# Optimization experiments

Hardware: AMD Instinct MI355X
Metric: run time of the kernel (lower is better)

Reference implementation:

```python
import jax, jax.numpy as jnp
import numpy as np

B, S, D, H = 2, 2048, 1024, 16
HD = D // H  # head_dim = 64


def setup_inputs() -> dict:
    key = jax.random.key(0)
    ks = jax.random.split(key, 11)
    s = 0.02  # keep projections well-scaled
    return {
        "Q": jax.random.normal(ks[0], (B, S, D), jnp.float32),
        "K": jax.random.normal(ks[1], (B, S, D), jnp.float32),
        "V": jax.random.normal(ks[2], (B, S, D), jnp.float32),
        "Wq": jax.random.normal(ks[3], (D, D), jnp.float32) * s,
        "bq": jax.random.normal(ks[4], (D,), jnp.float32) * s,
        "Wk": jax.random.normal(ks[5], (D, D), jnp.float32) * s,
        "bk": jax.random.normal(ks[6], (D,), jnp.float32) * s,
        "Wv": jax.random.normal(ks[7], (D, D), jnp.float32) * s,
        "bv": jax.random.normal(ks[8], (D,), jnp.float32) * s,
        "Wo": jax.random.normal(ks[9], (D, D), jnp.float32) * s,
        "bo": jax.random.normal(ks[10], (D,), jnp.float32) * s,
    }


def reference(Q, K, V, Wq, bq, Wk, bk, Wv, bv, Wo, bo):
    b, s, d = Q.shape
    # projections (torch Linear: x @ W.T + b)
    q = (Q @ Wq.T + bq).reshape(b, s, H, HD).transpose(0, 2, 1, 3)  # [B,H,S,HD]
    k = (K @ Wk.T + bk).reshape(b, s, H, HD).transpose(0, 2, 1, 3)
    v = (V @ Wv.T + bv).reshape(b, s, H, HD).transpose(0, 2, 1, 3)
    # scaled dot-product scores: [B,H,S,S]
    scale = 1.0 / jnp.sqrt(jnp.asarray(HD, q.dtype))
    scores = jnp.einsum("bhqd,bhkd->bhqk", q, k) * scale
    # module's explicit max-subtract before softmax
    scores = scores - jnp.max(scores, axis=-1, keepdims=True)
    attn = jax.nn.softmax(scores, axis=-1)
    # dropout p=0.0 (eval) -> identity; renormalize-after-dropout kept verbatim
    attn = attn / jnp.sum(attn, axis=-1, keepdims=True)
    ctx = jnp.einsum("bhqk,bhkd->bhqd", attn, v)  # [B,H,S,HD]
    ctx = ctx.transpose(0, 2, 1, 3).reshape(b, s, d)
    out = ctx @ Wo.T + bo
    return out
```

## Files before the change

kernel.cpp:

```cpp
#include <hip/hip_runtime.h>

#define SS 2048
#define SD 1024
#define SH 16
#define SHD 64
#define MROWS 4096
#define LOG2E 1.44269504088896340736f

typedef __attribute__((ext_vector_type(8))) short short8;
typedef __attribute__((ext_vector_type(4))) float floatx4;
typedef __attribute__((ext_vector_type(4))) unsigned short ushort4v;
typedef unsigned short u16;
typedef unsigned int u32;

#define AS1 __attribute__((address_space(1)))
#define AS3 __attribute__((address_space(3)))

__device__ inline u16 f2bf(float v) {
  u32 x = __builtin_bit_cast(u32, v);
  x = x + 0x7fffu + ((x >> 16) & 1u);
  return (u16)(x >> 16);
}

__global__ __launch_bounds__(256) void cast_all(
    const float* __restrict__ q, const float* __restrict__ k,
    const float* __restrict__ v, const float* __restrict__ wq,
    const float* __restrict__ wk, const float* __restrict__ wv,
    const float* __restrict__ wo, u16* __restrict__ out) {
  int i = blockIdx.x * 256 + threadIdx.x;
  const float* src;
  int idx;
  if (i < 3145728) {
    int a = i >> 20;
    src = (a == 0) ? q : ((a == 1) ? k : v);
    idx = i & 1048575;
  } else {
    int j = i - 3145728;
    int a = j >> 18;
    src = (a == 0) ? wq : ((a == 1) ? wk : ((a == 2) ? wv : wo));
    idx = j & 262143;
  }
  float4 f = ((const float4*)src)[idx];
  ushort4v o;
  o[0] = f2bf(f.x); o[1] = f2bf(f.y); o[2] = f2bf(f.z); o[3] = f2bf(f.w);
  ((ushort4v*)out)[i] = o;
}

__global__ __launch_bounds__(256, 3) void gemm_bt(
    const u16* __restrict__ Aall, const u16* __restrict__ Wall,
    const float* __restrict__ b0, const float* __restrict__ b1,
    const float* __restrict__ b2, u16* __restrict__ outb,
    float* __restrict__ outf, int mode, float qscale) {
  __shared__ u16 smem[16384];
  u16* lds_a = smem;
  u16* lds_w = smem + 8192;
  int z = blockIdx.z;
  const u16* A = Aall + (size_t)z * (MROWS * (size_t)SD);
  const u16* W = Wall + (size_t)z * (SD * (size_t)SD);
  const float* bias = (z == 0) ? b0 : ((z == 1) ? b1 : b2);
  float scale = (mode == 0 && z == 0) ? qscale : 1.0f;

  int tid = threadIdx.x;
  int lane = tid & 63, wave = tid >> 6;
  int l16 = lane & 15, quad = lane >> 4;
  int wm = (wave >> 1) * 64, wn = (wave & 1) * 64;
  int tm = blockIdx.y * 128, tn = blockIdx.x * 128;

  floatx4 acc[4][4];
  floatx4 zf = {0.f, 0.f, 0.f, 0.f};
#pragma unroll
  for (int r = 0; r < 4; r++)
#pragma unroll
    for (int c = 0; c < 4; c++) acc[r][c] = zf;

  const u16* pa[4];
  const u16* pw[4];
#pragma unroll
  for (int q = 0; q < 4; q++) {
    int srow = q * 32 + wave * 8 + (lane >> 3);
    int scol = (((lane & 7) ^ ((lane >> 3) & 7)) << 3);
    pa[q] = A + (size_t)(tm + srow) * SD + scol;
    pw[q] = W + (size_t)(tn + srow) * SD + scol;
  }

  for (int k0 = 0; k0 < SD; k0 += 64) {
#pragma unroll
    for (int q = 0; q < 4; q++) {
      __builtin_amdgcn_global_load_lds((const AS1 void*)pa[q],
          (AS3 void*)(AS3 u16*)&lds_a[(q * 32 + wave * 8) * 64], 16, 0, 0);
      __builtin_amdgcn_global_load_lds((const AS1 void*)pw[q],
          (AS3 void*)(AS3 u16*)&lds_w[(q * 32 + wave * 8) * 64], 16, 0, 0);
      pa[q] += 64; pw[q] += 64;
    }
    __syncthreads();
    short8 af[4][2], wf[4][2];
#pragma unroll
    for (int r = 0; r < 4; r++)
#pragma unroll
      for (int kk = 0; kk < 2; kk++)
        af[r][kk] = *(short8*)&lds_a[(wm + r * 16 + l16) * 64 +
                                     (((kk * 4 + quad) ^ (l16 & 7)) << 3)];
#pragma unroll
    for (int c = 0; c < 4; c++)
#pragma unroll
      for (int kk = 0; kk < 2; kk++)
        wf[c][kk] = *(short8*)&lds_w[(wn + c * 16 + l16) * 64 +
                                     (((kk * 4 + quad) ^ (l16 & 7)) << 3)];
#pragma unroll
    for (int r = 0; r < 4; r++)
#pragma unroll
      for (int c = 0; c < 4; c++) {
        acc[r][c] = __builtin_amdgcn_mfma_f32_16x16x32_bf16(af[r][0], wf[c][0], acc[r][c], 0, 0, 0);
        acc[r][c] = __builtin_amdgcn_mfma_f32_16x16x32_bf16(af[r][1], wf[c][1], acc[r][c], 0, 0, 0);
      }
    __syncthreads();
  }

  if (mode == 0) {
    u16* ob = outb + (size_t)z * (MROWS * (size_t)SD);
    if (z < 2) {
      u16* LT = smem;
#pragma unroll
      for (int r = 0; r < 4; r++) {
#pragma unroll
        for (int c = 0; c < 4; c++) {
          int feat = wn + c * 16 + l16;
          float bv = bias[tn + feat];
#pragma unroll
          for (int g = 0; g < 4; g++) {
            int key = wm + r * 16 + quad * 4 + g;
            float val = (acc[r][c][g] + bv) * scale;
            LT[key * 128 + ((((feat >> 3) ^ (key & 7)) << 3) | (feat & 7))] = f2bf(val);
          }
        }
      }
      __syncthreads();
      int bb = tm >> 11;
      int kt0 = (tm & 2047) >> 6;
#pragma unroll
      for (int i = 0; i < 8; i++) {
        int id = wave * 8 + i;
        int kt_rel = id >> 4, hrel = (id >> 3) & 1, ct = (id >> 1) & 3, hh = id & 1;
        int key = kt_rel * 64 + ct * 16 + l16;
        int chunk = hrel * 8 + hh * 4 + quad;
        short8 vv = *(short8*)&LT[key * 128 + ((chunk ^ (l16 & 7)) << 3)];
        int h = (tn >> 6) + hrel;
        u16* dst = ob + (size_t)(bb * SH + h) * (SS * SHD) +
                   ((kt0 + kt_rel) * 8 + ct * 2 + hh) * 512 + lane * 8;
        *(short8*)dst = vv;
      }
    } else {
      int h = (tn + wn) >> 6;
      int bb = (tm + wm) >> 11;
      int kt = ((tm + wm) & 2047) >> 6;
      u16* vbase = ob + (size_t)(bb * SH + h) * (SS * SHD) + (size_t)kt * 4096 +
                   (l16 * 4 + quad) * 8;
#pragma unroll
      for (int c = 0; c < 4; c++) {
        int gn = tn + wn + c * 16 + l16;
        float bv = bias[gn];
#pragma unroll
        for (int rp = 0; rp < 2; rp++) {
          union { u16 u[8]; short8 s; } pk;
#pragma unroll
          for (int g = 0; g < 4; g++) {
            pk.u[g]     = f2bf(acc[2 * rp][c][g] + bv);
            pk.u[4 + g] = f2bf(acc[2 * rp + 1][c][g] + bv);
          }
          *(short8*)&vbase[(c * 2 + rp) * 512] = pk.s;
        }
      }
    }
  } else {
#pragma unroll
    for (int r = 0; r < 4; r++) {
#pragma unroll
      for (int c = 0; c < 4; c++) {
        int gn = tn + wn + c * 16 + l16;
        float bv = bias[gn];
#pragma unroll
        for (int g = 0; g < 4; g++) {
          int gm = tm + wm + r * 16 + quad * 4 + g;
          outf[(size_t)gm * SD + gn] = acc[r][c][g] + bv;
        }
      }
    }
  }
}

__global__ __launch_bounds__(256, 2) void gemm_o(
    const u16* __restrict__ A, const u16* __restrict__ W,
    const float* __restrict__ bias, float* __restrict__ outf) {
  __shared__ u16 lds_a[64 * 64];
  __shared__ u16 lds_w[128 * 64];
  int tid = threadIdx.x;
  int lane = tid & 63, wave = tid >> 6;
  int l16 = lane & 15, quad = lane >> 4;
  int wm = (wave >> 1) * 32, wn = (wave & 1) * 64;
  int tm = blockIdx.y * 64, tn = blockIdx.x * 128;

  floatx4 acc[2][4];
  floatx4 zf = {0.f, 0.f, 0.f, 0.f};
#pragma unroll
  for (int r = 0; r < 2; r++)
#pragma unroll
    for (int c = 0; c < 4; c++) acc[r][c] = zf;

  int srow8 = wave * 8 + (lane >> 3);
  int scol = (((lane & 7) ^ ((lane >> 3) & 7)) << 3);
  const u16* pa[2];
  const u16* pw[4];
#pragma unroll
  for (int q = 0; q < 2; q++)
    pa[q] = A + (size_t)(tm + q * 32 + srow8) * SD + scol;
#pragma unroll
  for (int q = 0; q < 4; q++)
    pw[q] = W + (size_t)(tn + q * 32 + srow8) * SD + scol;

  for (int k0 = 0; k0 < SD; k0 += 64) {
#pragma unroll
    for (int q = 0; q < 2; q++) {
      __builtin_amdgcn_global_load_lds((const AS1 void*)pa[q],
          (AS3 void*)(AS3 u16*)&lds_a[(q * 32 + wave * 8) * 64], 16, 0, 0);
      pa[q] += 64;
    }
#pragma unroll
    for (int q = 0; q < 4; q++) {
      __builtin_amdgcn_global_load_lds((const AS1 void*)pw[q],
          (AS3 void*)(AS3 u16*)&lds_w[(q * 32 + wave * 8) * 64], 16, 0, 0);
      pw[q] += 64;
    }
    __syncthreads();
    short8 af[2][2], wf[4][2];
#pragma unroll
    for (int r = 0; r < 2; r++)
#pragma unroll
      for (int kk = 0; kk < 2; kk++)
        af[r][kk] = *(short8*)&lds_a[(wm + r * 16 + l16) * 64 +
                                     (((kk * 4 + quad) ^ (l16 & 7)) << 3)];
#pragma unroll
    for (int c = 0; c < 4; c++)
#pragma unroll
      for (int kk = 0; kk < 2; kk++)
        wf[c][kk] = *(short8*)&lds_w[(wn + c * 16 + l16) * 64 +
                                     (((kk * 4 + quad) ^ (l16 & 7)) << 3)];
#pragma unroll
    for (int r = 0; r < 2; r++)
#pragma unroll
      for (int c = 0; c < 4; c++) {
        acc[r][c] = __builtin_amdgcn_mfma_f32_16x16x32_bf16(af[r][0], wf[c][0], acc[r][c], 0, 0, 0);
        acc[r][c] = __builtin_amdgcn_mfma_f32_16x16x32_bf16(af[r][1], wf[c][1], acc[r][c], 0, 0, 0);
      }
    __syncthreads();
  }

#pragma unroll
  for (int r = 0; r < 2; r++) {
#pragma unroll
    for (int c = 0; c < 4; c++) {
      int gn = tn + wn + c * 16 + l16;
      float bv = bias[gn];
#pragma unroll
      for (int g = 0; g < 4; g++) {
        int gm = tm + wm + r * 16 + quad * 4 + g;
        outf[(size_t)gm * SD + gn] = acc[r][c][g] + bv;
      }
    }
  }
}

__global__ __launch_bounds__(128, 2) void attn(
    const u16* __restrict__ qb, const u16* __restrict__ kb,
    const u16* __restrict__ vfrag, u16* __restrict__ ctxb) {
  int lane = threadIdx.x & 63;
  int wave = threadIdx.x >> 6;
  int l16 = lane & 15, quad = lane >> 4;

  int raw = blockIdx.x;
  int xcd = raw & 7, slot = raw >> 3;
  int bh = xcd + 8 * (slot >> 5);
  int qt = slot & 31;
  int b = bh >> 4, h = bh & 15;
  int base = bh * (SS * SHD);
  int q0 = qt * 64;

  const u16* kp = kb + base + lane * 8;
  const u16* vp = vfrag + base + (l16 * 4 + quad) * 8;

  short8 qf[4][2];
#pragma unroll
  for (int t = 0; t < 4; t++)
#pragma unroll
    for (int hh = 0; hh < 2; hh++)
      qf[t][hh] = *(const short8*)&qb[base + (qt * 8 + t * 2 + hh) * 512 + lane * 8];

  floatx4 zf = {0.f, 0.f, 0.f, 0.f};
  floatx4 acc[4][4], accl[4];
#pragma unroll
  for (int t = 0; t < 4; t++) {
    accl[t] = zf;
#pragma unroll
    for (int c = 0; c < 4; c++) acc[t][c] = zf;
  }
  const short8 ones8 = {0x3F80, 0x3F80, 0x3F80, 0x3F80,
                        0x3F80, 0x3F80, 0x3F80, 0x3F80};

  int ktbase = wave * 16;
  short8 kf[4][2], vf[4][2];
  {
    const u16* p = kp + ktbase * 4096;
#pragma unroll
    for (int ct = 0; ct < 4; ct++)
#pragma unroll
      for (int hh = 0; hh < 2; hh++)
        kf[ct][hh] = *(const short8*)&p[(ct * 2 + hh) * 512];
    const u16* pv = vp + ktbase * 4096;
#pragma unroll
    for (int c = 0; c < 4; c++)
#pragma unroll
      for (int c2 = 0; c2 < 2; c2++)
        vf[c][c2] = *(const short8*)&pv[(c * 2 + c2) * 512];
  }

#pragma unroll 1
  for (int i = 0; i < 16; i++) {
    int nt = ktbase + ((i + 1) & 15);
    const u16* kpn = kp + nt * 4096;
    const u16* vpn = vp + nt * 4096;
#pragma unroll
    for (int c2 = 0; c2 < 2; c2++) {
      const int ct0 = 2 * c2, ct1 = 2 * c2 + 1;
      floatx4 se[4], so[4];
#pragma unroll
      for (int t = 0; t < 4; t++) {
        floatx4 zz = zf;
        zz = __builtin_amdgcn_mfma_f32_16x16x32_bf16(kf[ct0][0], qf[t][0], zz, 0, 0, 0);
        zz = __builtin_amdgcn_mfma_f32_16x16x32_bf16(kf[ct0][1], qf[t][1], zz, 0, 0, 0);
        se[t] = zz;
        floatx4 ww = zf;
        ww = __builtin_amdgcn_mfma_f32_16x16x32_bf16(kf[ct1][0], qf[t][0], ww, 0, 0, 0);
        ww = __builtin_amdgcn_mfma_f32_16x16x32_bf16(kf[ct1][1], qf[t][1], ww, 0, 0, 0);
        so[t] = ww;
      }
      kf[ct0][0] = *(const short8*)&kpn[(ct0 * 2 + 0) * 512];
      kf[ct0][1] = *(const short8*)&kpn[(ct0 * 2 + 1) * 512];
      kf[ct1][0] = *(const short8*)&kpn[(ct1 * 2 + 0) * 512];
      kf[ct1][1] = *(const short8*)&kpn[(ct1 * 2 + 1) * 512];
#pragma unroll
      for (int t = 0; t < 4; t++) {
        u32 e0 = __builtin_bit_cast(u32, __builtin_amdgcn_exp2f(se[t][0]));
        u32 e1 = __builtin_bit_cast(u32, __builtin_amdgcn_exp2f(se[t][1]));
        u32 e2 = __builtin_bit_cast(u32, __builtin_amdgcn_exp2f(se[t][2]));
        u32 e3 = __builtin_bit_cast(u32, __builtin_amdgcn_exp2f(se[t][3]));
        u32 o0 = __builtin_bit_cast(u32, __builtin_amdgcn_exp2f(so[t][0]));
        u32 o1 = __builtin_bit_cast(u32, __builtin_amdgcn_exp2f(so[t][1]));
        u32 o2 = __builtin_bit_cast(u32, __builtin_amdgcn_exp2f(so[t][2]));
        u32 o3 = __builtin_bit_cast(u32, __builtin_amdgcn_exp2f(so[t][3]));
        union { u32 u[4]; short8 s; } pa;
        pa.u[0] = __builtin_amdgcn_perm(e1, e0, 0x07060302);
        pa.u[1] = __builtin_amdgcn_perm(e3, e2, 0x07060302);
        pa.u[2] = __builtin_amdgcn_perm(o1, o0, 0x07060302);
        pa.u[3] = __builtin_amdgcn_perm(o3, o2, 0x07060302);
#pragma unroll
        for (int c = 0; c < 4; c++)
          acc[t][c] = __builtin_amdgcn_mfma_f32_16x16x32_bf16(pa.s, vf[c][c2], acc[t][c], 0, 0, 0);
        accl[t] = __builtin_amdgcn_mfma_f32_16x16x32_bf16(pa.s, ones8, accl[t], 0, 0, 0);
      }
#pragma unroll
      for (int c = 0; c < 4; c++)
        vf[c][c2] = *(const short8*)&vpn[(c * 2 + c2) * 512];
    }
  }

  __shared__ floatx4 red[2][64][11];
  int ow = 1 - wave;
#pragma unroll
  for (int t = 0; t < 4; t++) {
    if ((t >> 1) == ow) {
#pragma unroll
      for (int c = 0; c < 4; c++) red[ow][lane][(t & 1) * 5 + c] = acc[t][c];
      red[ow][lane][(t & 1) * 5 + 4] = accl[t];
    }
  }
  __syncthreads();
#pragma unroll
  for (int t = 0; t < 4; t++) {
    if ((t >> 1) == wave) {
#pragma unroll
      for (int c = 0; c < 4; c++) acc[t][c] += red[wave][lane][(t & 1) * 5 + c];
      accl[t] += red[wave][lane][(t & 1) * 5 + 4];
    }
  }

#pragma unroll
  for (int t = 0; t < 4; t++) {
    if ((t >> 1) == wave) {
#pragma unroll
      for (int g = 0; g < 4; g++) {
        float invg = 1.0f / accl[t][g];
        int qrow = q0 + t * 16 + quad * 4 + g;
#pragma unroll
        for (int c = 0; c < 4; c++) {
          int hd = c * 16 + l16;
          ctxb[(size_t)((b * SS + qrow) * SD + h * SHD + hd)] = f2bf(acc[t][c][g] * invg);
        }
      }
    }
  }
}

extern "C" void kernel_launch(void* const* d_in, const int* in_sizes, int n_in,
                              void* d_out, int out_size, void* d_ws, size_t ws_size,
                              hipStream_t stream) {
  const float* Q  = (const float*)d_in[0];
  const float* Kp = (const float*)d_in[1];
  const float* Vp = (const float*)d_in[2];
  const float* Wq = (const float*)d_in[3];
  const float* bq = (const float*)d_in[4];
  const float* Wk = (const float*)d_in[5];
  const float* bk = (const float*)d_in[6];
  const float* Wv = (const float*)d_in[7];
  const float* bv = (const float*)d_in[8];
  const float* Wo = (const float*)d_in[9];
  const float* bo = (const float*)d_in[10];

  u16* xb   = (u16*)d_ws;
  u16* wb   = xb + (size_t)3 * 4194304;
  u16* qkvb = wb + (size_t)4 * 1048576;
  u16* ctxb = qkvb + (size_t)3 * 4194304;
  float* out = (float*)d_out;

  cast_all<<<dim3(16384), dim3(256), 0, stream>>>(Q, Kp, Vp, Wq, Wk, Wv, Wo, xb);

  const float qscale = 0.125f * LOG2E;
  gemm_bt<<<dim3(8, 32, 3), dim3(256), 0, stream>>>(
      xb, wb, bq, bk, bv, qkvb, (float*)nullptr, 0, qscale);

  attn<<<dim3(1024), dim3(128), 0, stream>>>(
      qkvb, qkvb + (size_t)4194304, qkvb + (size_t)2 * 4194304, ctxb);

  gemm_o<<<dim3(8, 64), dim3(256), 0, stream>>>(
      ctxb, wb + (size_t)3 * 1048576, bo, out);
}
```

Baseline: 203.5 us.

## Software-pipeline attention loop so QK MFMAs overlap exp/pack of previous half-tile

Restructures the inner attention loop into a software pipeline: the exp/pack of one half-tile's scores is held in paA/paB while the next QK product and the PV accumulation of the prior half run, with a prologue and an epilogue. The aim is to interleave independent MFMA work with transcendental and VALU work so dependency stalls between the QK scores, the exp and the PV MFMA are hidden. The cost is more live registers (se/so plus two packed buffers), which may raise register pressure or lower occupancy, and reorders the V loads.

Measured after the change: 206.3 us. About the same (+1.4%).

```diff
diff --git a/kernel.cpp b/kernel.cpp
--- a/kernel.cpp
+++ b/kernel.cpp
@@ -307,70 +307,116 @@
 
   int ktbase = wave * 16;
   short8 kf[4][2], vf[4][2];
+  floatx4 se[4], so[4];
+  short8 paA[4], paB[4];
+
+#define QK_PAIR(CT0, CT1)                                                     \
+  do {                                                                        \
+    _Pragma("unroll")                                                         \
+    for (int t = 0; t < 4; t++) {                                             \
+      floatx4 zz = zf;                                                        \
+      zz = __builtin_amdgcn_mfma_f32_16x16x32_bf16(kf[CT0][0], qf[t][0], zz, 0, 0, 0); \
+      zz = __builtin_amdgcn_mfma_f32_16x16x32_bf16(kf[CT0][1], qf[t][1], zz, 0, 0, 0); \
+      se[t] = zz;                                                             \
+      floatx4 ww = zf;                                                        \
+      ww = __builtin_amdgcn_mfma_f32_16x16x32_bf16(kf[CT1][0], qf[t][0], ww, 0, 0, 0); \
+      ww = __builtin_amdgcn_mfma_f32_16x16x32_bf16(kf[CT1][1], qf[t][1], ww, 0, 0, 0); \
+      so[t] = ww;                                                             \
+    }                                                                         \
+  } while (0)
+
+#define PACK(PA)                                                              \
+  do {                                                                        \
+    _Pragma("unroll")                                                         \
+    for (int t = 0; t < 4; t++) {                                             \
+      u32 e0 = __builtin_bit_cast(u32, __builtin_amdgcn_exp2f(se[t][0]));     \
+      u32 e1 = __builtin_bit_cast(u32, __builtin_amdgcn_exp2f(se[t][1]));     \
+      u32 e2 = __builtin_bit_cast(u32, __builtin_amdgcn_exp2f(se[t][2]));     \
+      u32 e3 = __builtin_bit_cast(u32, __builtin_amdgcn_exp2f(se[t][3]));     \
+      u32 o0 = __builtin_bit_cast(u32, __builtin_amdgcn_exp2f(so[t][0]));     \
+      u32 o1 = __builtin_bit_cast(u32, __builtin_amdgcn_exp2f(so[t][1]));     \
+      u32 o2 = __builtin_bit_cast(u32, __builtin_amdgcn_exp2f(so[t][2]));     \
+      u32 o3 = __builtin_bit_cast(u32, __builtin_amdgcn_exp2f(so[t][3]));     \
+      union { u32 u[4]; short8 s; } pk;                                       \
+      pk.u[0] = __builtin_amdgcn_perm(e1, e0, 0x07060302);                    \
+      pk.u[1] = __builtin_amdgcn_perm(e3, e2, 0x07060302);                    \
+      pk.u[2] = __builtin_amdgcn_perm(o1, o0, 0x07060302);                    \
+      pk.u[3] = __builtin_amdgcn_perm(o3, o2, 0x07060302);                    \
+      PA[t] = pk.s;                                                           \
+    }                                                                         \
+  } while (0)
+
+#define PVACC(PA, C2)                                                         \
+  do {                                                                        \
+    _Pragma("unroll")                                                         \
+    for (int t = 0; t < 4; t++) {                                             \
+      _Pragma("unroll")                                                       \
+      for (int c = 0; c < 4; c++)                                             \
+        acc[t][c] = __builtin_amdgcn_mfma_f32_16x16x32_bf16(PA[t], vf[c][C2], acc[t][c], 0, 0, 0); \
+      accl[t] = __builtin_amdgcn_mfma_f32_16x16x32_bf16(PA[t], ones8, accl[t], 0, 0, 0); \
+    }                                                                         \
+  } while (0)
+
+#define LDK(PAIR, PTR)                                                        \
+  do {                                                                        \
+    kf[2*(PAIR)][0]   = *(const short8*)&(PTR)[(2*(PAIR)*2 + 0) * 512];       \
+    kf[2*(PAIR)][1]   = *(const short8*)&(PTR)[(2*(PAIR)*2 + 1) * 512];       \
+    kf[2*(PAIR)+1][0] = *(const short8*)&(PTR)[((2*(PAIR)+1)*2 + 0) * 512];   \
+    kf[2*(PAIR)+1][1] = *(const short8*)&(PTR)[((2*(PAIR)+1)*2 + 1) * 512];   \
+  } while (0)
+
+#define LDV(C2, PTR)                                                          \
+  do {                                                                        \
+    _Pragma("unroll")                                                         \
+    for (int c = 0; c < 4; c++)                                               \
+      vf[c][C2] = *(const short8*)&(PTR)[(c * 2 + (C2)) * 512];               \
+  } while (0)
+
+  LDK(0, kp + ktbase * 4096);
+  LDK(1, kp + ktbase * 4096);
+  LDV(0, vp + ktbase * 4096);
+
   {
-    const u16* p = kp + ktbase * 4096;
-#pragma unroll
-    for (int ct = 0; ct < 4; ct++)
-#pragma unroll
-      for (int hh = 0; hh < 2; hh++)
-        kf[ct][hh] = *(const short8*)&p[(ct * 2 + hh) * 512];
-    const u16* pv = vp + ktbase * 4096;
-#pragma unroll
-    for (int c = 0; c < 4; c++)
-#pragma unroll
-      for (int c2 = 0; c2 < 2; c2++)
-        vf[c][c2] = *(const short8*)&pv[(c * 2 + c2) * 512];
+    const u16* kpn = kp + (ktbase + 1) * 4096;
+    QK_PAIR(0, 1);
+    LDK(0, kpn);
+    LDV(1, vp + ktbase * 4096);
+    PACK(paA);
+  }
+  {
+    const u16* kpn = kp + (ktbase + 1) * 4096;
+    const u16* vpn = vp + (ktbase + 1) * 4096;
+    QK_PAIR(2, 3);
+    LDK(1, kpn);
+    PVACC(paA, 0);
+    LDV(0, vpn);
+    PACK(paB);
   }
 
 #pragma unroll 1
-  for (int i = 0; i < 16; i++) {
-    int nt = ktbase + ((i + 1) & 15);
+  for (int r = 1; r < 16; r++) {
+    int nt = ktbase + ((r + 1) & 15);
     const u16* kpn = kp + nt * 4096;
     const u16* vpn = vp + nt * 4096;
-#pragma unroll
-    for (int c2 = 0; c2 < 2; c2++) {
-      const int ct0 = 2 * c2, ct1 = 2 * c2 + 1;
-      floatx4 se[4], so[4];
-#pragma unroll
-      for (int t = 0; t < 4; t++) {
-        floatx4 zz = zf;
-        zz = __builtin_amdgcn_mfma_f32_16x16x32_bf16(kf[ct0][0], qf[t][0], zz, 0, 0, 0);
-        zz = __builtin_amdgcn_mfma_f32_16x16x32_bf16(kf[ct0][1], qf[t][1], zz, 0, 0, 0);
-        se[t] = zz;
-        floatx4 ww = zf;
-        ww = __builtin_amdgcn_mfma_f32_16x16x32_bf16(kf[ct1][0], qf[t][0], ww, 0, 0, 0);
-        ww = __builtin_amdgcn_mfma_f32_16x16x32_bf16(kf[ct1][1], qf[t][1], ww, 0, 0, 0);
-        so[t] = ww;
-      }
-      kf[ct0][0] = *(const short8*)&kpn[(ct0 * 2 + 0) * 512];
-      kf[ct0][1] = *(const short8*)&kpn[(ct0 * 2 + 1) * 512];
-      kf[ct1][0] = *(const short8*)&kpn[(ct1 * 2 + 0) * 512];
-      kf[ct1][1] = *(const short8*)&kpn[(ct1 * 2 + 1) * 512];
-#pragma unroll
-      for (int t = 0; t < 4; t++) {
-        u32 e0 = __builtin_bit_cast(u32, __builtin_amdgcn_exp2f(se[t][0]));
-        u32 e1 = __builtin_bit_cast(u32, __builtin_amdgcn_exp2f(se[t][1]));
-        u32 e2 = __builtin_bit_cast(u32, __builtin_amdgcn_exp2f(se[t][2]));
-        u32 e3 = __builtin_bit_cast(u32, __builtin_amdgcn_exp2f(se[t][3]));
-        u32 o0 = __builtin_bit_cast(u32, __builtin_amdgcn_exp2f(so[t][0]));
-        u32 o1 = __builtin_bit_cast(u32, __builtin_amdgcn_exp2f(so[t][1]));
-        u32 o2 = __builtin_bit_cast(u32, __builtin_amdgcn_exp2f(so[t][2]));
-        u32 o3 = __builtin_bit_cast(u32, __builtin_amdgcn_exp2f(so[t][3]));
-        union { u32 u[4]; short8 s; } pa;
-        pa.u[0] = __builtin_amdgcn_perm(e1, e0, 0x07060302);
-        pa.u[1] = __builtin_amdgcn_perm(e3, e2, 0x07060302);
-        pa.u[2] = __builtin_amdgcn_perm(o1, o0, 0x07060302);
-        pa.u[3] = __builtin_amdgcn_perm(o3, o2, 0x07060302);
-#pragma unroll
-        for (int c = 0; c < 4; c++)
-          acc[t][c] = __builtin_amdgcn_mfma_f32_16x16x32_bf16(pa.s, vf[c][c2], acc[t][c], 0, 0, 0);
-        accl[t] = __builtin_amdgcn_mfma_f32_16x16x32_bf16(pa.s, ones8, accl[t], 0, 0, 0);
-      }
-#pragma unroll
-      for (int c = 0; c < 4; c++)
-        vf[c][c2] = *(const short8*)&vpn[(c * 2 + c2) * 512];
-    }
-  }
+    const u16* vpc = vp + (ktbase + r) * 4096;
+    QK_PAIR(0, 1);
+    LDK(0, kpn);
+    PVACC(paB, 1);
+    LDV(1, vpc);
+    PACK(paA);
+    QK_PAIR(2, 3);
+    LDK(1, kpn);
+    PVACC(paA, 0);
+    LDV(0, vpn);
+    PACK(paB);
+  }
+  PVACC(paB, 1);
+
+#undef QK_PAIR
+#undef PACK
+#undef PVACC
+#undef LDK
+#undef LDV
 
   __shared__ floatx4 red[2][64][11];
   int ow = 1 - wave;
```
